# Optimization experiments

Hardware: AMD Instinct MI355X
Metric: run time of the kernel (lower is better)

## Reference

```python
import jax, jax.numpy as jnp
import numpy as np

N_PATCH = 676
K_SEL = int(676 * 0.8)  # 540
HEADS = 16
LN_EPS = 1e-5


def _layernorm(t, w, b):
    mu = t.mean(-1, keepdims=True)
    var = ((t - mu) ** 2).mean(-1, keepdims=True)
    return (t - mu) * jax.lax.rsqrt(var + LN_EPS) * w + b


def _attention(t, w_qkv, b_qkv, w_out, b_out):
    # t: [S, B, C] (seq-first, like torch nn.MultiheadAttention)
    S, B, C = t.shape
    D = C // HEADS
    qkv = t @ w_qkv.T + b_qkv                       # [S, B, 3C]
    q, k, v = jnp.split(qkv, 3, axis=-1)
    def heads(a):
        return a.reshape(S, B, HEADS, D).transpose(1, 2, 0, 3)  # [B,H,S,D]
    q, k, v = heads(q), heads(k), heads(v)
    scores = jnp.einsum('bhqd,bhkd->bhqk', q, k) / jnp.sqrt(jnp.asarray(D, t.dtype))
    attn = jax.nn.softmax(scores, axis=-1)
    o = jnp.einsum('bhqk,bhkd->bhqd', attn, v)      # [B,H,S,D]
    o = o.transpose(2, 0, 1, 3).reshape(S, B, C)
    return o @ w_out.T + b_out


def _mlp(t, w_fc1, b_fc1, w_fc2, b_fc2):
    h = t @ w_fc1.T + b_fc1
    h = h * jax.nn.sigmoid(1.702 * h)  # CLIP QuickGELU
    return h @ w_fc2.T + b_fc2


def setup_inputs() -> dict:
    key = jax.random.key(0)
    ks = jax.random.split(key, 6)
    C, B, L = 1024, 32, 77
    inp = {
        'x': jax.random.normal(ks[0], (1 + N_PATCH, B, C), jnp.float32),
        'lang_tokens': jax.random.normal(ks[1], (L, B, C), jnp.float32),
        'ln1_w': jnp.ones((C,), jnp.float32),
        'ln1_b': jnp.zeros((C,), jnp.float32),
        'ln2_w': jnp.ones((C,), jnp.float32),
        'ln2_b': jnp.zeros((C,), jnp.float32),
        'w_qkv': jax.random.normal(ks[2], (3 * C, C), jnp.float32) * 0.02,
        'b_qkv': jnp.zeros((3 * C,), jnp.float32),
        'w_out': jax.random.normal(ks[3], (C, C), jnp.float32) * 0.02,
        'b_out': jnp.zeros((C,), jnp.float32),
        'w_fc1': jax.random.normal(ks[4], (4 * C, C), jnp.float32) * 0.02,
        'b_fc1': jnp.zeros((4 * C,), jnp.float32),
        'w_fc2': jax.random.normal(ks[5], (C, 4 * C), jnp.float32) * 0.02,
        'b_fc2': jnp.zeros((C,), jnp.float32),
    }
    return inp


def reference(x, lang_tokens, ln1_w, ln1_b, ln2_w, ln2_b, w_qkv, b_qkv,
              w_out, b_out, w_fc1, b_fc1, w_fc2, b_fc2):
    Nfull, B, C = x.shape
    cls_x = x[:1]            # [1, B, C]
    xt = x[1:]               # [676, B, C]

    # per-token language-alignment score: [676, B]
    score = jnp.einsum('nbc,lbc->nbl', xt, lang_tokens).mean(-1)

    # top-k selection per batch column; torch boolean-mask gather preserves
    # the ORIGINAL token order within the high/low sets -> sort the indices.
    order = jnp.argsort(-score, axis=0)                 # descending
    high_idx = jnp.sort(order[:K_SEL], axis=0)          # [540, B]
    low_idx = jnp.sort(order[K_SEL:], axis=0)           # [136, B]

    delta_x = jnp.take_along_axis(xt, high_idx[:, :, None], axis=0)  # [540,B,C]
    low_x = jnp.take_along_axis(xt, low_idx[:, :, None], axis=0)     # [136,B,C]
    low_score = jnp.take_along_axis(score, low_idx, axis=0)[:, :, None]
    low_tok = (low_x * jax.nn.softmax(low_score, axis=0)).sum(0, keepdims=True)

    seq = jnp.concatenate([cls_x, delta_x, low_tok], axis=0)  # [542, B, C]
    d = _attention(_layernorm(seq, ln1_w, ln1_b), w_qkv, b_qkv, w_out, b_out)

    barange = jnp.arange(B)[None, :]
    temple = jnp.zeros_like(xt)
    temple = temple.at[high_idx, barange].set(d[1:-1])
    temple = temple.at[low_idx, barange].set(
        jnp.broadcast_to(d[-1:], (N_PATCH - K_SEL, B, C)))

    xt = xt + temple
    cls_x = cls_x + d[:1]
    x = jnp.concatenate([cls_x, xt], axis=0)
    x = x + _mlp(_layernorm(x, ln2_w, ln2_b), w_fc1, b_fc1, w_fc2, b_fc2)
    return x
```

## Files before the change

### kernel.cpp

```cpp
#include <hip/hip_runtime.h>
#include <hip/hip_bf16.h>

typedef unsigned short u16;
typedef __attribute__((ext_vector_type(4))) float f32x4;
typedef __attribute__((ext_vector_type(8))) short s16x8;

#define DEVI __device__ __forceinline__

static constexpr int NPATCH = 676;
static constexpr int KSEL   = 540;
static constexpr int NLOW   = 136;
static constexpr int BB     = 32;
static constexpr int CC     = 1024;
static constexpr int S      = 542;
static constexpr int SP     = 576;
static constexpr int M1P    = SP * BB;
static constexpr int NTOK   = 677;
static constexpr int M2     = NTOK * BB;
static constexpr int M2P    = 21760;
static constexpr int NKT    = SP / 64;
static constexpr int NQC    = 5;

DEVI u16 f2bf(float f) {
  unsigned u = __float_as_uint(f);
  u += 0x7fffu + ((u >> 16) & 1u);
  return (u16)(u >> 16);
}
DEVI float bf2f(u16 h) { return __uint_as_float(((unsigned)h) << 16); }
DEVI float ex2(float x) { float r; asm("v_exp_f32 %0, %1" : "=v"(r) : "v"(x)); return r; }

DEVI void gld16(const void* g, void* l) {
  __builtin_amdgcn_global_load_lds((const __attribute__((address_space(1))) void*)g,
                                   (__attribute__((address_space(3))) void*)l,
                                   16, 0, 0);
}

DEVI void BAR() {
  asm volatile("" ::: "memory");
  __builtin_amdgcn_s_barrier();
  asm volatile("" ::: "memory");
}
#define VMC(N) asm volatile("s_waitcnt vmcnt(" #N ")" ::: "memory")


__global__ void k_f2bf4(const float* __restrict__ in, u16* __restrict__ out, int n4) {
  int i = blockIdx.x * blockDim.x + threadIdx.x;
  if (i >= n4) return;
  float4 v = ((const float4*)in)[i];
  unsigned long long p = (unsigned long long)f2bf(v.x)
                       | ((unsigned long long)f2bf(v.y) << 16)
                       | ((unsigned long long)f2bf(v.z) << 32)
                       | ((unsigned long long)f2bf(v.w) << 48);
  *(unsigned long long*)&out[(long)i * 4] = p;
}

__global__ void k_langmean(const float* __restrict__ lang, float* __restrict__ lm) {
  int b = blockIdx.x, t = threadIdx.x;
  float a0 = 0, a1 = 0, a2 = 0, a3 = 0;
  for (int l = 0; l < 77; l++) {
    float4 v = ((const float4*)(lang + ((long)l * BB + b) * CC))[t];
    a0 += v.x; a1 += v.y; a2 += v.z; a3 += v.w;
  }
  const float inv = 1.f / 77.f;
  float4 o; o.x = a0 * inv; o.y = a1 * inv; o.z = a2 * inv; o.w = a3 * inv;
  ((float4*)(lm + b * CC))[t] = o;
}

__global__ void k_score(const float* __restrict__ x, const float* __restrict__ lm,
                        float* __restrict__ score) {
  int nb = blockIdx.x;
  int n = nb >> 5, b = nb & 31;
  int t = threadIdx.x;
  float4 xv = ((const float4*)(x + ((long)(n + 1) * BB + b) * CC))[t];
  float4 lv = ((const float4*)(lm + b * CC))[t];
  float s = xv.x * lv.x + xv.y * lv.y + xv.z * lv.z + xv.w * lv.w;
  for (int m = 1; m < 64; m <<= 1) s += __shfl_xor(s, m);
  __shared__ float sm[4];
  if ((t & 63) == 0) sm[t >> 6] = s;
  __syncthreads();
  if (t == 0) score[n * BB + b] = sm[0] + sm[1] + sm[2] + sm[3];
}

__global__ void k_select(const float* __restrict__ score, float* __restrict__ wall,
                         int* __restrict__ rowmap, int* __restrict__ selsrc,
                         int* __restrict__ lowlist) {
  int b = blockIdx.x, t = threadIdx.x;
  __shared__ float sc[NPATCH];
  __shared__ int hf[NPATCH];
  __shared__ float red[2];
  if (t < NPATCH) sc[t] = score[t * BB + b];
  __syncthreads();
  int high = 0;
  if (t < NPATCH) {
    float s = sc[t];
    int r = 0;
    for (int m = 0; m < NPATCH; m++) {
      float sm_ = sc[m];
      r += (sm_ > s) || (sm_ == s && m < t);
    }
    high = (r < KSEL);
    hf[t] = high;
  }
  __syncthreads();
  if (t < NPATCH) {
    int p = 0;
    for (int m = 0; m < t; m++) p += hf[m];
    if (high) {
      rowmap[b * NPATCH + t] = 1 + p;
      selsrc[b * S + 1 + p] = t + 1;
    } else {
      rowmap[b * NPATCH + t] = S - 1;
      lowlist[b * NLOW + (t - p)] = t;
    }
  }
  if (t == 0) selsrc[b * S + 0] = 0;
  __syncthreads();
  if (t == 0) {
    float m = -3e38f;
    for (int i = 0; i < NPATCH; i++) if (!hf[i]) m = fmaxf(m, sc[i]);
    float d = 0;
    for (int i = 0; i < NPATCH; i++) if (!hf[i]) d += __expf(sc[i] - m);
    red[0] = m; red[1] = d;
  }
  __syncthreads();
  if (t < NPATCH) wall[b * NPATCH + t] = hf[t] ? 0.f : __expf(sc[t] - red[0]) / red[1];
}

__global__ void k_lowtok(const float* __restrict__ x, const float* __restrict__ wall,
                         const int* __restrict__ lowlist, float* __restrict__ lowtok) {
  int b = blockIdx.x, ch = blockIdx.y;
  int c = ch * 256 + threadIdx.x;
  float acc = 0.f;
  for (int i = 0; i < NLOW; i++) {
    int n = lowlist[b * NLOW + i];
    acc += wall[b * NPATCH + n] * x[((long)(n + 1) * BB + b) * CC + c];
  }
  lowtok[b * CC + c] = acc;
}

__global__ void k_lnseq(const float* __restrict__ x, const float* __restrict__ lowtok,
                        const int* __restrict__ selsrc, const float* __restrict__ w,
                        const float* __restrict__ bias, u16* __restrict__ out) {
  int s = blockIdx.x, b = blockIdx.y, t = threadIdx.x;
  u16* orow = out + ((long)b * SP + s) * CC;
  if (s >= S) { *(unsigned long long*)&orow[4 * t] = 0ULL; return; }
  const float* src;
  if (s == 0)          src = x + (long)b * CC;
  else if (s == S - 1) src = lowtok + (long)b * CC;
  else                 src = x + ((long)selsrc[b * S + s] * BB + b) * CC;
  float4 v = ((const float4*)src)[t];
  float ss = v.x + v.y + v.z + v.w;
  float s2 = v.x * v.x + v.y * v.y + v.z * v.z + v.w * v.w;
  for (int k = 1; k < 64; k <<= 1) { ss += __shfl_xor(ss, k); s2 += __shfl_xor(s2, k); }
  __shared__ float sa[4], sb[4];
  if ((t & 63) == 0) { sa[t >> 6] = ss; sb[t >> 6] = s2; }
  __syncthreads();
  ss = sa[0] + sa[1] + sa[2] + sa[3];
  s2 = sb[0] + sb[1] + sb[2] + sb[3];
  float mu = ss * (1.f / CC);
  float var = s2 * (1.f / CC) - mu * mu;
  float rs = rsqrtf(var + 1e-5f);
  int c = 4 * t;
  unsigned long long p = (unsigned long long)f2bf((v.x - mu) * rs * w[c]     + bias[c])
                       | ((unsigned long long)f2bf((v.y - mu) * rs * w[c + 1] + bias[c + 1]) << 16)
                       | ((unsigned long long)f2bf((v.z - mu) * rs * w[c + 2] + bias[c + 2]) << 32)
                       | ((unsigned long long)f2bf((v.w - mu) * rs * w[c + 3] + bias[c + 3]) << 48);
  *(unsigned long long*)&orow[4 * t] = p;
}

__global__ void k_scatln(const float* __restrict__ x, const u16* __restrict__ dbuf,
                         const int* __restrict__ rowmap, const float* __restrict__ w,
                         const float* __restrict__ bias, float* __restrict__ out,
                         u16* __restrict__ lnout) {
  int m = blockIdx.x, t = threadIdx.x;
  u16* orow = lnout + (long)m * CC;
  if (m >= M2) { *(unsigned long long*)&orow[4 * t] = 0ULL; return; }
  int nf = m >> 5, b = m & 31;
  int srow = (nf == 0) ? 0 : rowmap[b * NPATCH + (nf - 1)];
  float4 xv = ((const float4*)(x + (long)m * CC))[t];
  unsigned long long dp = *(const unsigned long long*)&dbuf[((long)b * SP + srow) * CC + 4 * t];
  float4 v;
  v.x = xv.x + bf2f((u16)(dp));
  v.y = xv.y + bf2f((u16)(dp >> 16));
  v.z = xv.z + bf2f((u16)(dp >> 32));
  v.w = xv.w + bf2f((u16)(dp >> 48));
  ((float4*)(out + (long)m * CC))[t] = v;
  float ss = v.x + v.y + v.z + v.w;
  float s2 = v.x * v.x + v.y * v.y + v.z * v.z + v.w * v.w;
  for (int k = 1; k < 64; k <<= 1) { ss += __shfl_xor(ss, k); s2 += __shfl_xor(s2, k); }
  __shared__ float sa[4], sb[4];
  if ((t & 63) == 0) { sa[t >> 6] = ss; sb[t >> 6] = s2; }
  __syncthreads();
  ss = sa[0] + sa[1] + sa[2] + sa[3];
  s2 = sb[0] + sb[1] + sb[2] + sb[3];
  float mu = ss * (1.f / CC);
  float var = s2 * (1.f / CC) - mu * mu;
  float rs = rsqrtf(var + 1e-5f);
  int c = 4 * t;
  unsigned long long p = (unsigned long long)f2bf((v.x - mu) * rs * w[c]     + bias[c])
                       | ((unsigned long long)f2bf((v.y - mu) * rs * w[c + 1] + bias[c + 1]) << 16)
                       | ((unsigned long long)f2bf((v.z - mu) * rs * w[c + 2] + bias[c + 2]) << 32)
                       | ((unsigned long long)f2bf((v.w - mu) * rs * w[c + 3] + bias[c + 3]) << 48);
  *(unsigned long long*)&orow[4 * t] = p;
}


struct Epi {
  const float* bias;
  u16* obf;
  float* of;
  u16 *qb, *kb, *vtb;
  int mvalid, ldc;
};

DEVI void stage32(u16* dst, const u16* src, int ld) {
  int t = threadIdx.x;
#pragma unroll
  for (int q = 0; q < 2; q++) {
    int s = t + q * 256;
    int R = s >> 3, clp = s & 7;
    int lc = clp ^ (R & 7);
    int m = 2 * R + (lc >> 2), kc = lc & 3;
    gld16(src + (long)m * ld + kc * 8, dst + s * 8);
  }
}

DEVI s16x8 frag32(const u16* tile, int m, int h4) {
  int R = m >> 1;
  int phys = ((((m & 1) << 2) | h4) ^ (R & 7));
  return *(const s16x8*)(tile + R * 64 + phys * 8);
}

DEVI void stage64(u16* dst, const u16* src, int ld) {
  int t = threadIdx.x;
  int c = t & 7, r0 = t >> 3;
  gld16(src + (long)r0 * ld + ((c ^ (r0 & 7)) << 3), dst + t * 8);
  int r1 = r0 + 32;
  gld16(src + (long)r1 * ld + ((c ^ (r1 & 7)) << 3), dst + 2048 + t * 8);
}

DEVI s16x8 frag(const u16* half, int rh, int kk, int h4) {
  int chunk = ((kk << 2) | h4) ^ (rh & 7);
  return *(const s16x8*)(half + rh * 64 + chunk * 8);
}

template<int MODE>
__global__ __launch_bounds__(256, 3) void k_gemm5(const u16* __restrict__ A, int lda,
                                                  const u16* __restrict__ Bw, int ldb,
                                                  int K, Epi e) {
  __shared__ __align__(16) u16 lds[3][2][4096];
  int t = threadIdx.x;
  int lane = t & 63, w = t >> 6;
  int h4 = lane >> 4, r = lane & 15;
  int wr = w >> 1, wc = w & 1;
  int MBk = gridDim.x, NBk = gridDim.y;
  int nwg = MBk * NBk;
  int orig = blockIdx.y * MBk + blockIdx.x;
  int q8 = nwg >> 3, r8 = nwg & 7, xcd = orig & 7, rk = orig >> 3;
  int wgid = (xcd < r8 ? xcd * (q8 + 1) : r8 * (q8 + 1) + (xcd - r8) * q8) + rk;
  int bm = wgid / NBk, bn = wgid % NBk;

  const u16* Asrc = A + (long)bm * 128 * lda;
  const u16* Bsrc = Bw + (long)bn * 128 * ldb;
  int NT = K >> 5;

  f32x4 acc[4][4];
#pragma unroll
  for (int i = 0; i < 4; i++)
#pragma unroll
    for (int j = 0; j < 4; j++) acc[i][j] = {0.f, 0.f, 0.f, 0.f};

  stage32(lds[0][0], Asrc, lda);
  stage32(lds[0][1], Bsrc, ldb);
  if (NT > 1) {
    stage32(lds[1][0], Asrc + 32, lda);
    stage32(lds[1][1], Bsrc + 32, ldb);
  }

  int bufr = 0, bufw = 2;
  for (int kt = 0; kt < NT; kt++) {
    if (kt + 1 < NT) { VMC(4); } else { VMC(0); }
    BAR();
    if (kt + 2 < NT) {
      stage32(lds[bufw][0], Asrc + (kt + 2) * 32, lda);
      stage32(lds[bufw][1], Bsrc + (kt + 2) * 32, ldb);
    }
    const u16* At = lds[bufr][0];
    const u16* Bt = lds[bufr][1];
    s16x8 af[4], bf[4];
#pragma unroll
    for (int i = 0; i < 4; i++) af[i] = frag32(At, wr * 64 + i * 16 + r, h4);
#pragma unroll
    for (int j = 0; j < 4; j++) bf[j] = frag32(Bt, wc * 64 + j * 16 + r, h4);
#pragma unroll
    for (int i = 0; i < 4; i++)
#pragma unroll
      for (int j = 0; j < 4; j++)
        acc[i][j] = __builtin_amdgcn_mfma_f32_16x16x32_bf16(af[i], bf[j], acc[i][j], 0, 0, 0);
    bufr = (bufr == 2) ? 0 : bufr + 1;
    bufw = (bufw == 2) ? 0 : bufw + 1;
  }

  const float QSC = 0.125f * 1.44269504088896f;
#pragma unroll
  for (int i = 0; i < 4; i++) {
    int m0 = bm * 128 + wr * 64 + i * 16 + 4 * h4;
#pragma unroll
    for (int j = 0; j < 4; j++) {
      int n = bn * 128 + wc * 64 + j * 16 + r;
      float bias = (MODE == 3 && e.bias == nullptr) ? 0.f : e.bias[n];
      if (MODE == 0) {
        int part = n >> 10, cc = n & 1023;
        int hh = cc >> 6, dd = cc & 63;
        int b0 = m0 / SP, s0 = m0 % SP;
        if (part == 2) {
          u16 pk[4];
#pragma unroll
          for (int tt = 0; tt < 4; tt++) pk[tt] = f2bf(acc[i][j][tt] + bias);
          *(unsigned long long*)&e.vtb[((long)(b0 * 16 + hh) * 64 + dd) * SP + s0] =
              *(unsigned long long*)pk;
        } else {
          u16* dst = (part == 0 ? e.qb : e.kb) + ((long)(b0 * 16 + hh) * SP + s0) * 64 + dd;
          float scl = (part == 0) ? QSC : 1.f;
#pragma unroll
          for (int tt = 0; tt < 4; tt++) dst[tt * 64] = f2bf((acc[i][j][tt] + bias) * scl);
        }
      } else if (MODE == 1) {
#pragma unroll
        for (int tt = 0; tt < 4; tt++)
          e.obf[(long)(m0 + tt) * e.ldc + n] = f2bf(acc[i][j][tt] + bias);
      } else if (MODE == 2) {
#pragma unroll
        for (int tt = 0; tt < 4; tt++) {
          float v = acc[i][j][tt] + bias;
          v = v / (1.f + __expf(-1.702f * v));
          e.obf[(long)(m0 + tt) * e.ldc + n] = f2bf(v);
        }
      } else {
#pragma unroll
        for (int tt = 0; tt < 4; tt++) {
          int m = m0 + tt;
          if (m < e.mvalid) e.of[(long)m * CC + n] += acc[i][j][tt] + bias;
        }
      }
    }
  }
}


__global__ __launch_bounds__(256, 4) void k_attn2(const u16* __restrict__ qb,
                                                  const u16* __restrict__ kb,
                                                  const u16* __restrict__ vtb,
                                                  u16* __restrict__ aout) {
  __shared__ __align__(16) u16 Kt[2][4096];
  __shared__ __align__(16) u16 Vt[2][4096];
  __shared__ __align__(16) u16 Pl[4][1024];

  int nwg = gridDim.x;
  int orig = blockIdx.x;
  int q8 = nwg >> 3, r8 = nwg & 7, xcd = orig & 7, rk = orig >> 3;
  int wgid = (xcd < r8 ? xcd * (q8 + 1) : r8 * (q8 + 1) + (xcd - r8) * q8) + rk;
  int bh = wgid / NQC, qc = wgid % NQC;
  int b = bh >> 4, hh = bh & 15;
  int t = threadIdx.x, w = t >> 6, lane = t & 63;
  int h4 = lane >> 4, r = lane & 15;

  const u16* Q  = qb  + (long)bh * SP * 64;
  const u16* Kg = kb  + (long)bh * SP * 64;
  const u16* Vg = vtb + (long)bh * 64 * SP;

  int qt[2];
  bool act[2];
  s16x8 aq0[2], aq1[2];
  f32x4 o[2][4];
  float mM[2][4], lL[2][4];
#pragma unroll
  for (int sub = 0; sub < 2; sub++) {
    qt[sub] = qc * 8 + w * 2 + sub;
    act[sub] = qt[sub] < SP / 16;
    if (act[sub]) {
      aq0[sub] = *(const s16x8*)&Q[(qt[sub] * 16 + r) * 64 + h4 * 8];
      aq1[sub] = *(const s16x8*)&Q[(qt[sub] * 16 + r) * 64 + 32 + h4 * 8];
    }
#pragma unroll
    for (int i = 0; i < 4; i++) { o[sub][i] = {0.f, 0.f, 0.f, 0.f}; mM[sub][i] = -1e30f; lL[sub][i] = 0.f; }
  }

  stage64(Kt[0], Kg, 64);
  stage64(Vt[0], Vg, SP);
  VMC(0);
  BAR();

  for (int kt = 0; kt < NKT; kt++) {
    int cur = kt & 1;
    if (kt + 1 < NKT) {
      stage64(Kt[cur ^ 1], Kg + (kt + 1) * 64 * 64, 64);
      stage64(Vt[cur ^ 1], Vg + (kt + 1) * 64, SP);
    }
    int kv0 = kt * 64;
    const u16* Kc = Kt[cur];
    const u16* Vc = Vt[cur];
#pragma unroll
    for (int sub = 0; sub < 2; sub++) {
      if (!act[sub]) continue;
      f32x4 sf[4];
#pragma unroll
      for (int f = 0; f < 4; f++) {
        sf[f] = {0.f, 0.f, 0.f, 0.f};
        sf[f] = __builtin_amdgcn_mfma_f32_16x16x32_bf16(aq0[sub], frag(Kc, f * 16 + r, 0, h4), sf[f], 0, 0, 0);
        sf[f] = __builtin_amdgcn_mfma_f32_16x16x32_bf16(aq1[sub], frag(Kc, f * 16 + r, 1, h4), sf[f], 0, 0, 0);
      }
      if (kv0 + 64 > S) {
#pragma unroll
        for (int f = 0; f < 4; f++)
          if (kv0 + f * 16 + r >= S) {
#pragma unroll
            for (int tt = 0; tt < 4; tt++) sf[f][tt] = -1e30f;
          }
      }
      float mx[4];
#pragma unroll
      for (int tt = 0; tt < 4; tt++)
        mx[tt] = fmaxf(fmaxf(sf[0][tt], sf[1][tt]), fmaxf(sf[2][tt], sf[3][tt]));
      for (int msk = 1; msk < 16; msk <<= 1) {
#pragma unroll
        for (int tt = 0; tt < 4; tt++) mx[tt] = fmaxf(mx[tt], __shfl_xor(mx[tt], msk));
      }
      int need = 0;
#pragma unroll
      for (int tt = 0; tt < 4; tt++) need |= (mx[tt] > mM[sub][tt] + 8.f);
      if (__any(need)) {
#pragma unroll
        for (int tt = 0; tt < 4; tt++) {
          float mn = fmaxf(mM[sub][tt], mx[tt]);
          float sc = ex2(mM[sub][tt] - mn);
          mM[sub][tt] = mn;
          lL[sub][tt] *= sc;
#pragma unroll
          for (int nf = 0; nf < 4; nf++) o[sub][nf][tt] *= sc;
        }
      }
      float rs[4];
#pragma unroll
      for (int tt = 0; tt < 4; tt++) {
        float m_ = mM[sub][tt];
        float p0 = ex2(sf[0][tt] - m_), p1 = ex2(sf[1][tt] - m_);
        float p2 = ex2(sf[2][tt] - m_), p3 = ex2(sf[3][tt] - m_);
        sf[0][tt] = p0; sf[1][tt] = p1; sf[2][tt] = p2; sf[3][tt] = p3;
        rs[tt] = (p0 + p1) + (p2 + p3);
      }
      for (int msk = 1; msk < 16; msk <<= 1) {
#pragma unroll
        for (int tt = 0; tt < 4; tt++) rs[tt] += __shfl_xor(rs[tt], msk);
      }
#pragma unroll
      for (int tt = 0; tt < 4; tt++) lL[sub][tt] += rs[tt];
      u16* Pw = Pl[w];
#pragma unroll
      for (int f = 0; f < 4; f++)
#pragma unroll
        for (int tt = 0; tt < 4; tt++) {
          int q = 4 * h4 + tt;
          int chunk = (f * 2 + (r >> 3)) ^ (q & 7);
          Pw[q * 64 + chunk * 8 + (r & 7)] = f2bf(sf[f][tt]);
        }
      s16x8 pa0 = frag(Pw, r, 0, h4);
      s16x8 pa1 = frag(Pw, r, 1, h4);
#pragma unroll
      for (int nf = 0; nf < 4; nf++) {
        o[sub][nf] = __builtin_amdgcn_mfma_f32_16x16x32_bf16(pa0, frag(Vc, nf * 16 + r, 0, h4), o[sub][nf], 0, 0, 0);
        o[sub][nf] = __builtin_amdgcn_mfma_f32_16x16x32_bf16(pa1, frag(Vc, nf * 16 + r, 1, h4), o[sub][nf], 0, 0, 0);
      }
    }
    VMC(0);
    BAR();
  }

#pragma unroll
  for (int sub = 0; sub < 2; sub++) {
    if (!act[sub]) continue;
    float inv[4];
#pragma unroll
    for (int tt = 0; tt < 4; tt++) inv[tt] = 1.f / lL[sub][tt];
#pragma unroll
    for (int nf = 0; nf < 4; nf++)
#pragma unroll
      for (int tt = 0; tt < 4; tt++) {
        int q = qt[sub] * 16 + 4 * h4 + tt;
        if (q < S) aout[((long)b * SP + q) * CC + hh * 64 + nf * 16 + r] = f2bf(o[sub][nf][tt] * inv[tt]);
      }
  }
}


extern "C" void kernel_launch(void* const* d_in, const int* in_sizes, int n_in,
                              void* d_out, int out_size, void* d_ws, size_t ws_size,
                              hipStream_t stream) {
  const float* x    = (const float*)d_in[0];
  const float* lang = (const float*)d_in[1];
  const float* ln1w = (const float*)d_in[2];
  const float* ln1b = (const float*)d_in[3];
  const float* ln2w = (const float*)d_in[4];
  const float* ln2b = (const float*)d_in[5];
  const float* wqkv = (const float*)d_in[6];
  const float* bqkv = (const float*)d_in[7];
  const float* wout = (const float*)d_in[8];
  const float* bout = (const float*)d_in[9];
  const float* wfc1 = (const float*)d_in[10];
  const float* bfc1 = (const float*)d_in[11];
  const float* wfc2 = (const float*)d_in[12];
  const float* bfc2 = (const float*)d_in[13];
  float* out = (float*)d_out;
  char* ws = (char*)d_ws;
  const size_t MiB = 1ull << 20;

  float* lm      = (float*)(ws + 0 * MiB);
  float* score   = (float*)(ws + 1 * MiB);
  float* wall    = (float*)(ws + 2 * MiB);
  int*   rowmap  = (int*)  (ws + 3 * MiB);
  int*   selsrc  = (int*)  (ws + 4 * MiB);
  int*   lowlist = (int*)  (ws + 5 * MiB);
  float* lowtok  = (float*)(ws + 6 * MiB);
  u16* wqb  = (u16*)(ws + 7 * MiB);
  u16* wob  = (u16*)(ws + 13 * MiB);
  u16* wf1b = (u16*)(ws + 15 * MiB);
  u16* wf2b = (u16*)(ws + 23 * MiB);
  u16* qbuf = (u16*)(ws + 31 * MiB);
  u16* kbuf = (u16*)(ws + 67 * MiB);
  u16* vtb  = (u16*)(ws + 103 * MiB);
  u16* regA = (u16*)(ws + 139 * MiB);
  u16* lnseq = regA;
  u16* aout  = regA;
  u16* dbuf  = vtb;
  u16* ln2bf = qbuf;
  u16* hbuf  = (u16*)(ws + 74 * MiB);

  {
    int n4;
    n4 = 3072 * 1024 / 4; k_f2bf4<<<(n4 + 255) / 256, 256, 0, stream>>>(wqkv, wqb, n4);
    n4 = 1024 * 1024 / 4; k_f2bf4<<<(n4 + 255) / 256, 256, 0, stream>>>(wout, wob, n4);
    n4 = 4096 * 1024 / 4; k_f2bf4<<<(n4 + 255) / 256, 256, 0, stream>>>(wfc1, wf1b, n4);
    n4 = 1024 * 4096 / 4; k_f2bf4<<<(n4 + 255) / 256, 256, 0, stream>>>(wfc2, wf2b, n4);
  }

  k_langmean<<<BB, 256, 0, stream>>>(lang, lm);
  k_score<<<NPATCH * BB, 256, 0, stream>>>(x, lm, score);
  k_select<<<BB, 1024, 0, stream>>>(score, wall, rowmap, selsrc, lowlist);
  k_lowtok<<<dim3(BB, 4), 256, 0, stream>>>(x, wall, lowlist, lowtok);
  k_lnseq<<<dim3(SP, BB), 256, 0, stream>>>(x, lowtok, selsrc, ln1w, ln1b, lnseq);

  {
    Epi e = {};
    e.bias = bqkv; e.qb = qbuf; e.kb = kbuf; e.vtb = vtb; e.mvalid = M1P;
    k_gemm5<0><<<dim3(M1P / 128, 3072 / 128), 256, 0, stream>>>(lnseq, 1024, wqb, 1024, 1024, e);
  }

  k_attn2<<<BB * 16 * NQC, 256, 0, stream>>>(qbuf, kbuf, vtb, aout);

  {
    Epi e = {};
    e.bias = bout; e.obf = dbuf; e.mvalid = M1P; e.ldc = 1024;
    k_gemm5<1><<<dim3(M1P / 128, 1024 / 128), 256, 0, stream>>>(aout, 1024, wob, 1024, 1024, e);
  }

  k_scatln<<<M2P, 256, 0, stream>>>(x, dbuf, rowmap, ln2w, ln2b, out, ln2bf);

  for (int c = 0; c < 2; c++) {
    Epi e2 = {};
    e2.bias = bfc1 + c * 2048; e2.obf = hbuf; e2.mvalid = M2P; e2.ldc = 2048;
    k_gemm5<2><<<dim3(M2P / 128, 2048 / 128), 256, 0, stream>>>(ln2bf, 1024, wf1b + (long)c * 2048 * 1024, 1024, 1024, e2);
    Epi e3 = {};
    e3.bias = (c == 0 ? bfc2 : nullptr); e3.of = out; e3.mvalid = M2;
    k_gemm5<3><<<dim3(M2P / 128, 1024 / 128), 256, 0, stream>>>(hbuf, 2048, wf2b + c * 2048, 4096, 2048, e3);
  }
}
```

Before: 1.098 ms.

## Add 128x256-tile GEMM kernel for QKV and FC1 projections

Adds a second GEMM kernel that computes a 128x256 output tile per workgroup, with each wave owning a 64x128 sub-tile. It uses double-buffered LDS staging with a barrier per k-step, in place of the previous triple-buffer scheme. The QKV and FC1 GEMMs move to it, which raises arithmetic intensity per LDS load and halves the number of workgroups. In exchange it doubles the accumulator registers, lowering occupancy to 2 workgroups per CU, and loses a stage of prefetch depth. The epilogue is factored into a shared helper.

```diff
diff --git a/kernel.cpp b/kernel.cpp
--- a/kernel.cpp
+++ b/kernel.cpp
@@ -245,6 +245,46 @@
 }
 
 template<int MODE>
+DEVI void epi_store(const Epi& e, int m0, int n, const f32x4& a, float bias) {
+  const float QSC = 0.125f * 1.44269504088896f;
+  if (MODE == 0) {
+    int part = n >> 10, cc = n & 1023;
+    int hh = cc >> 6, dd = cc & 63;
+    int b0 = m0 / SP, s0 = m0 % SP;
+    if (part == 2) {
+      u16 pk[4];
+#pragma unroll
+      for (int tt = 0; tt < 4; tt++) pk[tt] = f2bf(a[tt] + bias);
+      *(unsigned long long*)&e.vtb[((long)(b0 * 16 + hh) * 64 + dd) * SP + s0] =
+          *(unsigned long long*)pk;
+    } else {
+      u16* dst = (part == 0 ? e.qb : e.kb) + ((long)(b0 * 16 + hh) * SP + s0) * 64 + dd;
+      float scl = (part == 0) ? QSC : 1.f;
+#pragma unroll
+      for (int tt = 0; tt < 4; tt++) dst[tt * 64] = f2bf((a[tt] + bias) * scl);
+    }
+  } else if (MODE == 1) {
+#pragma unroll
+    for (int tt = 0; tt < 4; tt++)
+      e.obf[(long)(m0 + tt) * e.ldc + n] = f2bf(a[tt] + bias);
+  } else if (MODE == 2) {
+#pragma unroll
+    for (int tt = 0; tt < 4; tt++) {
+      float v = a[tt] + bias;
+      v = v / (1.f + __expf(-1.702f * v));
+      e.obf[(long)(m0 + tt) * e.ldc + n] = f2bf(v);
+    }
+  } else {
+#pragma unroll
+    for (int tt = 0; tt < 4; tt++) {
+      int m = m0 + tt;
+      if (m < e.mvalid) e.of[(long)m * CC + n] += a[tt] + bias;
+    }
+  }
+}
+
+
+template<int MODE>
 __global__ __launch_bounds__(256, 3) void k_gemm5(const u16* __restrict__ A, int lda,
                                                   const u16* __restrict__ Bw, int ldb,
                                                   int K, Epi e) {
@@ -301,7 +341,6 @@
     bufw = (bufw == 2) ? 0 : bufw + 1;
   }
 
-  const float QSC = 0.125f * 1.44269504088896f;
 #pragma unroll
   for (int i = 0; i < 4; i++) {
     int m0 = bm * 128 + wr * 64 + i * 16 + 4 * h4;
@@ -309,40 +348,73 @@
     for (int j = 0; j < 4; j++) {
       int n = bn * 128 + wc * 64 + j * 16 + r;
       float bias = (MODE == 3 && e.bias == nullptr) ? 0.f : e.bias[n];
-      if (MODE == 0) {
-        int part = n >> 10, cc = n & 1023;
-        int hh = cc >> 6, dd = cc & 63;
-        int b0 = m0 / SP, s0 = m0 % SP;
-        if (part == 2) {
-          u16 pk[4];
-#pragma unroll
-          for (int tt = 0; tt < 4; tt++) pk[tt] = f2bf(acc[i][j][tt] + bias);
-          *(unsigned long long*)&e.vtb[((long)(b0 * 16 + hh) * 64 + dd) * SP + s0] =
-              *(unsigned long long*)pk;
-        } else {
-          u16* dst = (part == 0 ? e.qb : e.kb) + ((long)(b0 * 16 + hh) * SP + s0) * 64 + dd;
-          float scl = (part == 0) ? QSC : 1.f;
-#pragma unroll
-          for (int tt = 0; tt < 4; tt++) dst[tt * 64] = f2bf((acc[i][j][tt] + bias) * scl);
-        }
-      } else if (MODE == 1) {
-#pragma unroll
-        for (int tt = 0; tt < 4; tt++)
-          e.obf[(long)(m0 + tt) * e.ldc + n] = f2bf(acc[i][j][tt] + bias);
-      } else if (MODE == 2) {
-#pragma unroll
-        for (int tt = 0; tt < 4; tt++) {
-          float v = acc[i][j][tt] + bias;
-          v = v / (1.f + __expf(-1.702f * v));
-          e.obf[(long)(m0 + tt) * e.ldc + n] = f2bf(v);
-        }
-      } else {
-#pragma unroll
-        for (int tt = 0; tt < 4; tt++) {
-          int m = m0 + tt;
-          if (m < e.mvalid) e.of[(long)m * CC + n] += acc[i][j][tt] + bias;
-        }
-      }
+      epi_store<MODE>(e, m0, n, acc[i][j], bias);
+    }
+  }
+}
+
+
+template<int MODE>
+__global__ __launch_bounds__(256, 2) void k_gemm6(const u16* __restrict__ A, int lda,
+                                                  const u16* __restrict__ Bw, int ldb,
+                                                  int K, Epi e) {
+  __shared__ __align__(16) u16 lds[2][3][4096];
+  int t = threadIdx.x;
+  int lane = t & 63, w = t >> 6;
+  int h4 = lane >> 4, r = lane & 15;
+  int wr = w >> 1, wc = w & 1;
+  int MBk = gridDim.x, NBk = gridDim.y;
+  int nwg = MBk * NBk;
+  int orig = blockIdx.y * MBk + blockIdx.x;
+  int q8 = nwg >> 3, r8 = nwg & 7, xcd = orig & 7, rk = orig >> 3;
+  int wgid = (xcd < r8 ? xcd * (q8 + 1) : r8 * (q8 + 1) + (xcd - r8) * q8) + rk;
+  int bm = wgid / NBk, bn = wgid % NBk;
+
+  const u16* Asrc = A + (long)bm * 128 * lda;
+  const u16* Bsrc = Bw + (long)bn * 256 * ldb;
+  int NT = K >> 5;
+
+  f32x4 acc[4][8];
+#pragma unroll
+  for (int i = 0; i < 4; i++)
+#pragma unroll
+    for (int j = 0; j < 8; j++) acc[i][j] = {0.f, 0.f, 0.f, 0.f};
+
+  stage32(lds[0][0], Asrc, lda);
+  stage32(lds[0][1], Bsrc, ldb);
+  stage32(lds[0][2], Bsrc + (long)128 * ldb, ldb);
+  __syncthreads();
+
+  for (int kt = 0; kt < NT; kt++) {
+    int cur = kt & 1;
+    if (kt + 1 < NT) {
+      stage32(lds[cur ^ 1][0], Asrc + (kt + 1) * 32, lda);
+      stage32(lds[cur ^ 1][1], Bsrc + (kt + 1) * 32, ldb);
+      stage32(lds[cur ^ 1][2], Bsrc + (long)128 * ldb + (kt + 1) * 32, ldb);
+    }
+    const u16* At = lds[cur][0];
+    const u16* Bt = lds[cur][1 + wc];
+    s16x8 af[4], bf[8];
+#pragma unroll
+    for (int i = 0; i < 4; i++) af[i] = frag32(At, wr * 64 + i * 16 + r, h4);
+#pragma unroll
+    for (int j = 0; j < 8; j++) bf[j] = frag32(Bt, j * 16 + r, h4);
+#pragma unroll
+    for (int i = 0; i < 4; i++)
+#pragma unroll
+      for (int j = 0; j < 8; j++)
+        acc[i][j] = __builtin_amdgcn_mfma_f32_16x16x32_bf16(af[i], bf[j], acc[i][j], 0, 0, 0);
+    __syncthreads();
+  }
+
+#pragma unroll
+  for (int i = 0; i < 4; i++) {
+    int m0 = bm * 128 + wr * 64 + i * 16 + 4 * h4;
+#pragma unroll
+    for (int j = 0; j < 8; j++) {
+      int n = bn * 256 + wc * 128 + j * 16 + r;
+      float bias = (MODE == 3 && e.bias == nullptr) ? 0.f : e.bias[n];
+      epi_store<MODE>(e, m0, n, acc[i][j], bias);
     }
   }
 }
@@ -552,7 +624,7 @@
   {
     Epi e = {};
     e.bias = bqkv; e.qb = qbuf; e.kb = kbuf; e.vtb = vtb; e.mvalid = M1P;
-    k_gemm5<0><<<dim3(M1P / 128, 3072 / 128), 256, 0, stream>>>(lnseq, 1024, wqb, 1024, 1024, e);
+    k_gemm6<0><<<dim3(M1P / 128, 3072 / 256), 256, 0, stream>>>(lnseq, 1024, wqb, 1024, 1024, e);
   }
 
   k_attn2<<<BB * 16 * NQC, 256, 0, stream>>>(qbuf, kbuf, vtb, aout);
@@ -568,7 +640,7 @@
   for (int c = 0; c < 2; c++) {
     Epi e2 = {};
     e2.bias = bfc1 + c * 2048; e2.obf = hbuf; e2.mvalid = M2P; e2.ldc = 2048;
-    k_gemm5<2><<<dim3(M2P / 128, 2048 / 128), 256, 0, stream>>>(ln2bf, 1024, wf1b + (long)c * 2048 * 1024, 1024, 1024, e2);
+    k_gemm6<2><<<dim3(M2P / 128, 2048 / 256), 256, 0, stream>>>(ln2bf, 1024, wf1b + (long)c * 2048 * 1024, 1024, 1024, e2);
     Epi e3 = {};
     e3.bias = (c == 0 ? bfc2 : nullptr); e3.of = out; e3.mvalid = M2;
     k_gemm5<3><<<dim3(M2P / 128, 1024 / 128), 256, 0, stream>>>(hbuf, 2048, wf2b + c * 2048, 4096, 2048, e3);
```

Measured after the change: 1.102 ms. Within noise of the previous version (+0.3%).
